# Performance work log

Hardware: AMD Instinct MI355X
Metric: run time of the kernel (lower is better)

Reference implementation:

```python
import jax, jax.numpy as jnp
import numpy as np

NUM_Q, NUM_P = 8192, 4096


def setup_inputs() -> dict:
    key = jax.random.key(0)
    k1, k2 = jax.random.split(key)
    pred = jax.random.normal(k1, (NUM_Q, NUM_P), dtype=jnp.float32)
    y = jax.random.randint(k2, (NUM_Q, NUM_P), 0, 2, dtype=jnp.int32)
    # guarantee every query has at least one relevant passage (argwhere(y==1) nonempty)
    y = y.at[:, 0].set(1)
    return {"pred": pred, "y": y}


def reference(pred, y):
    # Per row: comparer = min of pred over relevant (y==1) entries.
    # MarginRankingLoss(margin=0, reduction='mean') with target=(y!=1):
    #   target==1 (non-relevant): max(0, -(comparer - pred_j)) = relu(pred_j - min_rlv)
    #   target==0 (relevant):     max(0, 0) = 0
    rlv = (y == 1)
    min_rlv = jnp.min(jnp.where(rlv, pred, jnp.inf), axis=1, keepdims=True)  # [Q,1]
    hinge = jnp.where(rlv, 0.0, jnp.maximum(pred - min_rlv, 0.0))            # [Q,P]
    per_q = hinge.mean(axis=1)                                               # [Q]
    return per_q.mean()
```

## Files before the change

kernel.cpp:

```cpp
#include <hip/hip_runtime.h>
#include <float.h>

#define NUM_Q 8192
#define NUM_P 4096

__global__ __launch_bounds__(256)
void mmrl_kernel(const float* __restrict__ pred,
                 const int* __restrict__ y,
                 float* __restrict__ ws) {
    const int row = blockIdx.x;
    const int t = threadIdx.x;

    const float4* prow = reinterpret_cast<const float4*>(pred + (size_t)row * NUM_P);
    const int4*   yrow = reinterpret_cast<const int4*>(y + (size_t)row * NUM_P);

    float4 pv[4];
    int4   yv[4];
#pragma unroll
    for (int i = 0; i < 4; ++i) {
        pv[i] = prow[t + 256 * i];
        yv[i] = yrow[t + 256 * i];
    }

    float lmin = FLT_MAX;
#pragma unroll
    for (int i = 0; i < 4; ++i) {
        if (yv[i].x == 1) lmin = fminf(lmin, pv[i].x);
        if (yv[i].y == 1) lmin = fminf(lmin, pv[i].y);
        if (yv[i].z == 1) lmin = fminf(lmin, pv[i].z);
        if (yv[i].w == 1) lmin = fminf(lmin, pv[i].w);
    }
#pragma unroll
    for (int off = 32; off > 0; off >>= 1)
        lmin = fminf(lmin, __shfl_xor(lmin, off));

    __shared__ float smin[4];
    __shared__ float ssum[4];
    const int wave = t >> 6;
    if ((t & 63) == 0) smin[wave] = lmin;
    __syncthreads();
    const float rmin = fminf(fminf(smin[0], smin[1]), fminf(smin[2], smin[3]));

    float lsum = 0.0f;
#pragma unroll
    for (int i = 0; i < 4; ++i) {
        if (yv[i].x != 1) lsum += fmaxf(pv[i].x - rmin, 0.0f);
        if (yv[i].y != 1) lsum += fmaxf(pv[i].y - rmin, 0.0f);
        if (yv[i].z != 1) lsum += fmaxf(pv[i].z - rmin, 0.0f);
        if (yv[i].w != 1) lsum += fmaxf(pv[i].w - rmin, 0.0f);
    }
#pragma unroll
    for (int off = 32; off > 0; off >>= 1)
        lsum += __shfl_xor(lsum, off);

    if ((t & 63) == 0) ssum[wave] = lsum;
    __syncthreads();

    if (t == 0) {
        ws[row] = (ssum[0] + ssum[1]) + (ssum[2] + ssum[3]);
    }
}

__global__ __launch_bounds__(256)
void mmrl_reduce_kernel(const float* __restrict__ partial,
                        float* __restrict__ out) {
    const int t = threadIdx.x;
    const float4* p4 = reinterpret_cast<const float4*>(partial);
    float s = 0.0f;
#pragma unroll
    for (int i = 0; i < 8; ++i) {
        float4 v = p4[t + 256 * i];
        s += (v.x + v.y) + (v.z + v.w);
    }
#pragma unroll
    for (int off = 32; off > 0; off >>= 1)
        s += __shfl_xor(s, off);

    __shared__ float ss[4];
    if ((t & 63) == 0) ss[t >> 6] = s;
    __syncthreads();

    if (t == 0) {
        const float total = (ss[0] + ss[1]) + (ss[2] + ss[3]);
        out[0] = total * (1.0f / ((float)NUM_Q * (float)NUM_P));
    }
}

extern "C" void kernel_launch(void* const* d_in, const int* in_sizes, int n_in,
                              void* d_out, int out_size, void* d_ws, size_t ws_size,
                              hipStream_t stream) {
    const float* pred = (const float*)d_in[0];
    const int*   y    = (const int*)d_in[1];
    float* out = (float*)d_out;
    float* ws  = (float*)d_ws;

    mmrl_kernel<<<NUM_Q, 256, 0, stream>>>(pred, y, ws);
    mmrl_reduce_kernel<<<1, 256, 0, stream>>>(ws, out);
}
```

Measured before the change: 268.0 us.

## Assign one wavefront per row and pack relevance labels into bitmasks

Each 64-lane wavefront now handles a whole row, so a block covers four rows and the shared-memory min/sum exchanges and both __syncthreads disappear; the min and sum reductions use only wave shuffles. The int labels are compressed into two 32-bit masks per lane so that only the 16 float4 prediction vectors stay live in registers, and launch bounds request 4 blocks per CU. This removes block-level synchronization and aims for more independent loads in flight per wave, at the cost of higher register pressure and fewer blocks.

```diff
diff --git a/kernel.cpp b/kernel.cpp
--- a/kernel.cpp
+++ b/kernel.cpp
@@ -4,61 +4,72 @@
 #define NUM_Q 8192
 #define NUM_P 4096
 
-__global__ __launch_bounds__(256)
+__global__ __launch_bounds__(256, 4)
 void mmrl_kernel(const float* __restrict__ pred,
                  const int* __restrict__ y,
                  float* __restrict__ ws) {
-    const int row = blockIdx.x;
-    const int t = threadIdx.x;
+    const int lane = threadIdx.x & 63;
+    const int row  = blockIdx.x * (256 >> 6) + (threadIdx.x >> 6);
 
     const float4* prow = reinterpret_cast<const float4*>(pred + (size_t)row * NUM_P);
     const int4*   yrow = reinterpret_cast<const int4*>(y + (size_t)row * NUM_P);
 
-    float4 pv[4];
-    int4   yv[4];
+    float4 pv[16];
 #pragma unroll
-    for (int i = 0; i < 4; ++i) {
-        pv[i] = prow[t + 256 * i];
-        yv[i] = yrow[t + 256 * i];
+    for (int i = 0; i < 16; ++i) pv[i] = prow[lane + 64 * i];
+
+    unsigned int m0 = 0u, m1 = 0u;
+    {
+        int4 ya[8];
+#pragma unroll
+        for (int i = 0; i < 8; ++i) ya[i] = yrow[lane + 64 * i];
+#pragma unroll
+        for (int i = 0; i < 8; ++i) {
+            unsigned int b = (unsigned int)(ya[i].x == 1)
+                           | ((unsigned int)(ya[i].y == 1) << 1)
+                           | ((unsigned int)(ya[i].z == 1) << 2)
+                           | ((unsigned int)(ya[i].w == 1) << 3);
+            m0 |= b << (4 * i);
+        }
+#pragma unroll
+        for (int i = 0; i < 8; ++i) ya[i] = yrow[lane + 64 * (8 + i)];
+#pragma unroll
+        for (int i = 0; i < 8; ++i) {
+            unsigned int b = (unsigned int)(ya[i].x == 1)
+                           | ((unsigned int)(ya[i].y == 1) << 1)
+                           | ((unsigned int)(ya[i].z == 1) << 2)
+                           | ((unsigned int)(ya[i].w == 1) << 3);
+            m1 |= b << (4 * i);
+        }
     }
 
     float lmin = FLT_MAX;
 #pragma unroll
-    for (int i = 0; i < 4; ++i) {
-        if (yv[i].x == 1) lmin = fminf(lmin, pv[i].x);
-        if (yv[i].y == 1) lmin = fminf(lmin, pv[i].y);
-        if (yv[i].z == 1) lmin = fminf(lmin, pv[i].z);
-        if (yv[i].w == 1) lmin = fminf(lmin, pv[i].w);
+    for (int i = 0; i < 16; ++i) {
+        const unsigned int m = (i < 8) ? (m0 >> (4 * i)) : (m1 >> (4 * (i - 8)));
+        lmin = fminf(lmin, (m & 1u) ? pv[i].x : FLT_MAX);
+        lmin = fminf(lmin, (m & 2u) ? pv[i].y : FLT_MAX);
+        lmin = fminf(lmin, (m & 4u) ? pv[i].z : FLT_MAX);
+        lmin = fminf(lmin, (m & 8u) ? pv[i].w : FLT_MAX);
     }
 #pragma unroll
     for (int off = 32; off > 0; off >>= 1)
         lmin = fminf(lmin, __shfl_xor(lmin, off));
 
-    __shared__ float smin[4];
-    __shared__ float ssum[4];
-    const int wave = t >> 6;
-    if ((t & 63) == 0) smin[wave] = lmin;
-    __syncthreads();
-    const float rmin = fminf(fminf(smin[0], smin[1]), fminf(smin[2], smin[3]));
-
     float lsum = 0.0f;
 #pragma unroll
-    for (int i = 0; i < 4; ++i) {
-        if (yv[i].x != 1) lsum += fmaxf(pv[i].x - rmin, 0.0f);
-        if (yv[i].y != 1) lsum += fmaxf(pv[i].y - rmin, 0.0f);
-        if (yv[i].z != 1) lsum += fmaxf(pv[i].z - rmin, 0.0f);
-        if (yv[i].w != 1) lsum += fmaxf(pv[i].w - rmin, 0.0f);
+    for (int i = 0; i < 16; ++i) {
+        const unsigned int m = (i < 8) ? (m0 >> (4 * i)) : (m1 >> (4 * (i - 8)));
+        lsum += (m & 1u) ? 0.0f : fmaxf(pv[i].x - lmin, 0.0f);
+        lsum += (m & 2u) ? 0.0f : fmaxf(pv[i].y - lmin, 0.0f);
+        lsum += (m & 4u) ? 0.0f : fmaxf(pv[i].z - lmin, 0.0f);
+        lsum += (m & 8u) ? 0.0f : fmaxf(pv[i].w - lmin, 0.0f);
     }
 #pragma unroll
     for (int off = 32; off > 0; off >>= 1)
         lsum += __shfl_xor(lsum, off);
 
-    if ((t & 63) == 0) ssum[wave] = lsum;
-    __syncthreads();
-
-    if (t == 0) {
-        ws[row] = (ssum[0] + ssum[1]) + (ssum[2] + ssum[3]);
-    }
+    if (lane == 0) ws[row] = lsum;
 }
 
 __global__ __launch_bounds__(256)
@@ -94,6 +105,6 @@
     float* out = (float*)d_out;
     float* ws  = (float*)d_ws;
 
-    mmrl_kernel<<<NUM_Q, 256, 0, stream>>>(pred, y, ws);
+    mmrl_kernel<<<NUM_Q / 4, 256, 0, stream>>>(pred, y, ws);
     mmrl_reduce_kernel<<<1, 256, 0, stream>>>(ws, out);
 }
```

New measurement: 273.4 us. No clear change (+2.0%).
